# Kernel tuning notes

Hardware: AMD Instinct MI355X
Metric: run time of the kernel (lower is better)

## Reference

```python
import jax, jax.numpy as jnp
import numpy as np

AIR_TOKENS = jnp.array([102, 576, 3352], dtype=jnp.int32)
VOCAB = 3717
PS = 4  # patch size
L_CONN, L_PATCH, L_SMOOTH, L_SUPPORT = 0.5, 0.3, 0.1, 0.2


def _non_air(structure):
    # [B,X,Y,Z] bool: True where block is not air
    return ~jnp.isin(structure, AIR_TOKENS)


def connectivity_loss(structure):
    na = _non_air(structure).astype(jnp.float32)  # [B,X,Y,Z]
    p = jnp.pad(na, ((0, 0), (1, 1), (1, 1), (1, 1)))
    # 6-neighbor count (face adjacency), same math as the conv3d kernel
    neighbors = (p[:, :-2, 1:-1, 1:-1] + p[:, 2:, 1:-1, 1:-1]
                 + p[:, 1:-1, :-2, 1:-1] + p[:, 1:-1, 2:, 1:-1]
                 + p[:, 1:-1, 1:-1, :-2] + p[:, 1:-1, 1:-1, 2:])
    isolated = (neighbors == 0) & (na > 0)
    return isolated.astype(jnp.float32).sum() / (na.sum() + 1e-6)


def patch_consistency_loss(structure):
    B, X, Y, Z = structure.shape
    nx, ny, nz = X // PS, Y // PS, Z // PS
    num_patches = nx * ny * nz
    # [B, nx, PS, ny, PS, nz, PS] -> [B*num_patches, PS^3]
    patches = structure.reshape(B, nx, PS, ny, PS, nz, PS)
    patches = patches.transpose(0, 1, 3, 5, 2, 4, 6).reshape(B * num_patches, PS ** 3)
    P = B * num_patches
    # per-patch histogram over the vocab (fused replacement for unique/count loop)
    counts = jnp.zeros((P, VOCAB), jnp.float32)
    counts = counts.at[jnp.arange(P)[:, None], patches].add(1.0)
    counts = counts.at[:, AIR_TOKENS].set(0.0)  # drop air tokens
    s = counts.sum(-1, keepdims=True)
    probs = counts / jnp.maximum(s, 1.0)  # all-air patches -> probs 0 -> entropy 0
    entropy = -(probs * jnp.log(probs + 1e-10)).sum()
    return entropy / (B * num_patches + 1e-6)


def support_loss(structure):
    na = _non_air(structure)  # [B,X,Y,Z], Y is vertical
    support_below = jnp.concatenate(
        [jnp.ones_like(na[:, :, :1, :]), na[:, :, :-1, :]], axis=2)
    unsupported = na & ~support_below
    unsupported = unsupported.at[:, :, 0, :].set(False)  # exclude bottom layer
    return unsupported.astype(jnp.float32).sum() / (na.astype(jnp.float32).sum() + 1e-6)


def smoothness_loss(emb):
    # emb: [B, C, X, Y, Z]
    dx = jnp.abs(emb[:, :, 1:, :, :] - emb[:, :, :-1, :, :]).mean()
    dy = jnp.abs(emb[:, :, :, 1:, :] - emb[:, :, :, :-1, :]).mean()
    dz = jnp.abs(emb[:, :, :, :, 1:] - emb[:, :, :, :, :-1]).mean()
    return (dx + dy + dz) / 3.0


def setup_inputs() -> dict:
    key = jax.random.key(0)
    k1, k2 = jax.random.split(key)
    structure = jax.random.randint(k1, (64, 32, 32, 32), 0, VOCAB, dtype=jnp.int32)
    block_embeddings = jax.random.normal(k2, (64, 32, 32, 32, 32), dtype=jnp.float32)
    return {"structure": structure, "block_embeddings": block_embeddings}


def reference(structure, block_embeddings):
    l_conn = connectivity_loss(structure)
    l_patch = patch_consistency_loss(structure)
    l_support = support_loss(structure)
    l_smooth = smoothness_loss(block_embeddings)
    total = (L_CONN * l_conn + L_PATCH * l_patch
             + L_SMOOTH * l_smooth + L_SUPPORT * l_support)
    return (total, l_conn, l_patch, l_smooth, l_support)
```

## Files before the change

kernel.cpp:

```cpp
#include <hip/hip_runtime.h>


#define SM_BLOCKS 2048
#define ST_BLOCKS 1024
#define PA_BLOCKS 512
#define WS_DX  0
#define WS_DY  (SM_BLOCKS)
#define WS_DZ  (2 * SM_BLOCKS)
#define WS_ISO (3 * SM_BLOCKS)
#define WS_NA  (WS_ISO + ST_BLOCKS)
#define WS_UNS (WS_NA + ST_BLOCKS)
#define WS_ENT (WS_UNS + ST_BLOCKS)

__device__ __forceinline__ bool non_air(int t) {
    return !(t == 102 || t == 576 || t == 3352);
}

__device__ __forceinline__ double wave_red_d(double v) {
    #pragma unroll
    for (int off = 32; off > 0; off >>= 1) v += __shfl_down(v, off, 64);
    return v;
}
__device__ __forceinline__ float wave_red_f(float v) {
    #pragma unroll
    for (int off = 32; off > 0; off >>= 1) v += __shfl_down(v, off, 64);
    return v;
}
__device__ __forceinline__ int wave_red_i(int v) {
    #pragma unroll
    for (int off = 32; off > 0; off >>= 1) v += __shfl_down(v, off, 64);
    return v;
}

__device__ void smooth_body(const float4* __restrict__ e4,
                            double* __restrict__ part, int bid) {
    double adx = 0.0, ady = 0.0, adz = 0.0;
    const int stride = SM_BLOCKS * 256;
    for (int idx4 = bid * 256 + (int)threadIdx.x; idx4 < (1 << 24); idx4 += stride) {
        const int z4 = idx4 & 7;
        const int y = (idx4 >> 3) & 31;
        const int x = (idx4 >> 8) & 31;

        const float4 v = e4[idx4];

        const float nxt = __shfl_down(v.x, 1, 64);
        float dz = fabsf(v.y - v.x) + fabsf(v.z - v.y) + fabsf(v.w - v.z);
        if (z4 < 7) dz += fabsf(nxt - v.w);

        float dy = 0.0f;
        if (y < 31) {
            const float4 n = e4[idx4 + 8];
            dy = fabsf(n.x - v.x) + fabsf(n.y - v.y) + fabsf(n.z - v.z) + fabsf(n.w - v.w);
        }
        float dx = 0.0f;
        if (x < 31) {
            const float4 n = e4[idx4 + 256];
            dx = fabsf(n.x - v.x) + fabsf(n.y - v.y) + fabsf(n.z - v.z) + fabsf(n.w - v.w);
        }
        adx += dx; ady += dy; adz += dz;
    }

    adx = wave_red_d(adx); ady = wave_red_d(ady); adz = wave_red_d(adz);
    __shared__ double sm[3][4];
    const int lane = threadIdx.x & 63, wid = threadIdx.x >> 6;
    if (lane == 0) { sm[0][wid] = adx; sm[1][wid] = ady; sm[2][wid] = adz; }
    __syncthreads();
    if (threadIdx.x == 0) {
        part[WS_DX + bid] = sm[0][0] + sm[0][1] + sm[0][2] + sm[0][3];
        part[WS_DY + bid] = sm[1][0] + sm[1][1] + sm[1][2] + sm[1][3];
        part[WS_DZ + bid] = sm[2][0] + sm[2][1] + sm[2][2] + sm[2][3];
    }
}

__device__ void struct_body(const int* __restrict__ s,
                            double* __restrict__ part, int bid) {
    int iso = 0, nai = 0, unsup = 0;
    const int stride = ST_BLOCKS * 256;
    for (int idx = bid * 256 + (int)threadIdx.x; idx < (1 << 21); idx += stride) {
        const int z = idx & 31;
        const int y = (idx >> 5) & 31;
        const int x = (idx >> 10) & 31;
        const int t = s[idx];
        if (non_air(t)) {
            ++nai;
            int ncnt = 0;
            bool below = false;
            if (x > 0)  ncnt += non_air(s[idx - 1024]);
            if (x < 31) ncnt += non_air(s[idx + 1024]);
            if (y > 0)  { below = non_air(s[idx - 32]); ncnt += below; }
            if (y < 31) ncnt += non_air(s[idx + 32]);
            if (z > 0)  ncnt += non_air(s[idx - 1]);
            if (z < 31) ncnt += non_air(s[idx + 1]);
            iso += (ncnt == 0);
            unsup += (y > 0 && !below);
        }
    }
    iso = wave_red_i(iso); nai = wave_red_i(nai); unsup = wave_red_i(unsup);
    __shared__ int sm[3][4];
    const int lane = threadIdx.x & 63, wid = threadIdx.x >> 6;
    if (lane == 0) { sm[0][wid] = iso; sm[1][wid] = nai; sm[2][wid] = unsup; }
    __syncthreads();
    if (threadIdx.x == 0) {
        part[WS_ISO + bid] = (double)(sm[0][0] + sm[0][1] + sm[0][2] + sm[0][3]);
        part[WS_NA  + bid] = (double)(sm[1][0] + sm[1][1] + sm[1][2] + sm[1][3]);
        part[WS_UNS + bid] = (double)(sm[2][0] + sm[2][1] + sm[2][2] + sm[2][3]);
    }
}

__device__ void patch_body(const int* __restrict__ s,
                           double* __restrict__ part, int bid) {
    const int lane = threadIdx.x & 63, wid = threadIdx.x >> 6;
    const int gwave = bid * 4 + wid;
    const int nwaves = PA_BLOCKS * 4;
    const int px = lane >> 4, py = (lane >> 2) & 3, pz = lane & 3;

    float esum = 0.0f;
    for (int pid = gwave; pid < 32768; pid += nwaves) {
        const int b = pid >> 9;
        const int rem = pid & 511;
        const int ix = rem >> 6, iy = (rem >> 3) & 7, iz = rem & 7;
        const int x = ix * 4 + px, y = iy * 4 + py, z = iz * 4 + pz;

        const int t = s[((b * 32 + x) * 32 + y) * 32 + z];
        const bool na = non_air(t);
        const int scount = __popcll(__ballot(na));

        int c = 0, minj = 64;
        #pragma unroll 8
        for (int j = 0; j < 64; ++j) {
            const int tj = __shfl(t, j, 64);
            if (tj == t) { ++c; if (j < minj) minj = j; }
        }
        if (na && minj == lane) {
            const float p = (float)c / (float)(scount > 1 ? scount : 1);
            esum += -p * logf(p + 1e-10f);
        }
    }
    const float w = wave_red_f(esum);
    __shared__ float smp[4];
    if (lane == 0) smp[wid] = w;
    __syncthreads();
    if (threadIdx.x == 0)
        part[WS_ENT + bid] = (double)(smp[0] + smp[1] + smp[2] + smp[3]);
}

__global__ __launch_bounds__(256) void fused_kernel(const int* __restrict__ s,
                                                    const float4* __restrict__ e4,
                                                    double* __restrict__ part) {
    const int bid = blockIdx.x;
    if (bid < SM_BLOCKS) {
        smooth_body(e4, part, bid);
    } else if (bid < SM_BLOCKS + ST_BLOCKS) {
        struct_body(s, part, bid - SM_BLOCKS);
    } else {
        patch_body(s, part, bid - SM_BLOCKS - ST_BLOCKS);
    }
}

__global__ __launch_bounds__(256) void finalize_kernel(const double* __restrict__ part,
                                                       float* __restrict__ out) {
    __shared__ double sm[4];
    __shared__ double res[7];
    const int lane = threadIdx.x & 63, wid = threadIdx.x >> 6;
    const int base[7] = {WS_DX, WS_DY, WS_DZ, WS_ISO, WS_NA, WS_UNS, WS_ENT};
    const int len[7]  = {SM_BLOCKS, SM_BLOCKS, SM_BLOCKS, ST_BLOCKS, ST_BLOCKS, ST_BLOCKS, PA_BLOCKS};
    for (int k = 0; k < 7; ++k) {
        double a = 0.0;
        for (int i = threadIdx.x; i < len[k]; i += 256) a += part[base[k] + i];
        a = wave_red_d(a);
        if (lane == 0) sm[wid] = a;
        __syncthreads();
        if (threadIdx.x == 0) res[k] = sm[0] + sm[1] + sm[2] + sm[3];
        __syncthreads();
    }
    if (threadIdx.x == 0) {
        const double na = res[4];
        const double l_conn    = res[3] / (na + 1e-6);
        const double l_support = res[5] / (na + 1e-6);
        const double l_patch   = res[6] / (32768.0 + 1e-6);
        const double nd = 65011712.0;
        const double l_smooth  = (res[0] / nd + res[1] / nd + res[2] / nd) / 3.0;
        const double total = 0.5 * l_conn + 0.3 * l_patch + 0.1 * l_smooth + 0.2 * l_support;
        out[0] = (float)total;
        out[1] = (float)l_conn;
        out[2] = (float)l_patch;
        out[3] = (float)l_smooth;
        out[4] = (float)l_support;
    }
}

extern "C" void kernel_launch(void* const* d_in, const int* in_sizes, int n_in,
                              void* d_out, int out_size, void* d_ws, size_t ws_size,
                              hipStream_t stream) {
    const int*   s   = (const int*)d_in[0];
    const float* emb = (const float*)d_in[1];
    float* out   = (float*)d_out;
    double* part = (double*)d_ws;

    fused_kernel<<<SM_BLOCKS + ST_BLOCKS + PA_BLOCKS, 256, 0, stream>>>(
        s, (const float4*)emb, part);
    finalize_kernel<<<1, 256, 0, stream>>>(part, out);
}
```

Before: 437.6 us.

## Restructure smoothness loop with fixed trip count, float accumulators, and reordered block roles

The smoothness pass now uses a fixed 16-iteration loop that processes two float4 elements per iteration with branchless neighbor offsets. It reads the z-neighbor directly from memory instead of using a wave shuffle, and accumulates in float rather than double. The structure loop gets a constant trip count, and the structure and patch block counts are halved. Blocks are reordered so the slower patch and structure work is scheduled first. This should cut per-iteration index math and double-precision adds and give more memory-level parallelism, at the cost of float accumulation precision and fewer blocks for the integer passes.

```diff
diff --git a/kernel.cpp b/kernel.cpp
--- a/kernel.cpp
+++ b/kernel.cpp
@@ -2,8 +2,8 @@
 
 
 #define SM_BLOCKS 2048
-#define ST_BLOCKS 1024
-#define PA_BLOCKS 512
+#define ST_BLOCKS 512
+#define PA_BLOCKS 256
 #define WS_DX  0
 #define WS_DY  (SM_BLOCKS)
 #define WS_DZ  (2 * SM_BLOCKS)
@@ -32,38 +32,52 @@
     return v;
 }
 
-__device__ void smooth_body(const float4* __restrict__ e4,
+__device__ __forceinline__ float sad4(float4 a, float4 b) {
+    return fabsf(a.x - b.x) + fabsf(a.y - b.y) + fabsf(a.z - b.z) + fabsf(a.w - b.w);
+}
+
+__device__ void smooth_body(const float* __restrict__ e,
+                            const float4* __restrict__ e4,
                             double* __restrict__ part, int bid) {
-    double adx = 0.0, ady = 0.0, adz = 0.0;
-    const int stride = SM_BLOCKS * 256;
-    for (int idx4 = bid * 256 + (int)threadIdx.x; idx4 < (1 << 24); idx4 += stride) {
-        const int z4 = idx4 & 7;
-        const int y = (idx4 >> 3) & 31;
-        const int x = (idx4 >> 8) & 31;
-
-        const float4 v = e4[idx4];
-
-        const float nxt = __shfl_down(v.x, 1, 64);
-        float dz = fabsf(v.y - v.x) + fabsf(v.z - v.y) + fabsf(v.w - v.z);
-        if (z4 < 7) dz += fabsf(nxt - v.w);
-
-        float dy = 0.0f;
-        if (y < 31) {
-            const float4 n = e4[idx4 + 8];
-            dy = fabsf(n.x - v.x) + fabsf(n.y - v.y) + fabsf(n.z - v.z) + fabsf(n.w - v.w);
-        }
-        float dx = 0.0f;
-        if (x < 31) {
-            const float4 n = e4[idx4 + 256];
-            dx = fabsf(n.x - v.x) + fabsf(n.y - v.y) + fabsf(n.z - v.z) + fabsf(n.w - v.w);
-        }
-        adx += dx; ady += dy; adz += dz;
-    }
-
-    adx = wave_red_d(adx); ady = wave_red_d(ady); adz = wave_red_d(adz);
+    const int t0 = bid * 256 + (int)threadIdx.x;
+    const int z4 = t0 & 7;
+    const int y  = (t0 >> 3) & 31;
+    const int x  = (t0 >> 8) & 31;
+    const int   oy  = (y < 31) ? 8 : 0;
+    const int   ox  = (x < 31) ? 256 : 0;
+    const int   oz  = (z4 < 7) ? 4 : 0;
+    const float mzf = (z4 < 7) ? 1.0f : 0.0f;
+
+    float ax = 0.0f, ay = 0.0f, az = 0.0f;
+    const int S = 1 << 19;
+
+    #pragma unroll 1
+    for (int k = 0; k < 32; k += 2) {
+        const int i0 = t0 + k * S;
+        const int i1 = i0 + S;
+        const float4 v0 = e4[i0];
+        const float4 v1 = e4[i1];
+        const float4 py0 = e4[i0 + oy];
+        const float4 py1 = e4[i1 + oy];
+        const float4 px0 = e4[i0 + ox];
+        const float4 px1 = e4[i1 + ox];
+        const float  f0 = e[(i0 << 2) + oz];
+        const float  f1 = e[(i1 << 2) + oz];
+
+        az += fabsf(v0.y - v0.x) + fabsf(v0.z - v0.y) + fabsf(v0.w - v0.z)
+            + mzf * fabsf(f0 - v0.w);
+        az += fabsf(v1.y - v1.x) + fabsf(v1.z - v1.y) + fabsf(v1.w - v1.z)
+            + mzf * fabsf(f1 - v1.w);
+        ay += sad4(py0, v0) + sad4(py1, v1);
+        ax += sad4(px0, v0) + sad4(px1, v1);
+    }
+
+    double dxd = wave_red_d((double)ax);
+    double dyd = wave_red_d((double)ay);
+    double dzd = wave_red_d((double)az);
     __shared__ double sm[3][4];
     const int lane = threadIdx.x & 63, wid = threadIdx.x >> 6;
-    if (lane == 0) { sm[0][wid] = adx; sm[1][wid] = ady; sm[2][wid] = adz; }
+    if (lane == 0) { sm[0][wid] = dxd; sm[1][wid] = dyd; sm[2][wid] = dzd; }
     __syncthreads();
     if (threadIdx.x == 0) {
         part[WS_DX + bid] = sm[0][0] + sm[0][1] + sm[0][2] + sm[0][3];
@@ -74,12 +88,12 @@
 
 __device__ void struct_body(const int* __restrict__ s,
                             double* __restrict__ part, int bid) {
+    const int t0 = bid * 256 + (int)threadIdx.x;
+    const int z = t0 & 31, y = (t0 >> 5) & 31, x = (t0 >> 10) & 31;
     int iso = 0, nai = 0, unsup = 0;
-    const int stride = ST_BLOCKS * 256;
-    for (int idx = bid * 256 + (int)threadIdx.x; idx < (1 << 21); idx += stride) {
-        const int z = idx & 31;
-        const int y = (idx >> 5) & 31;
-        const int x = (idx >> 10) & 31;
+    #pragma unroll 2
+    for (int k = 0; k < 16; ++k) {
+        const int idx = t0 + (k << 17);
         const int t = s[idx];
         if (non_air(t)) {
             ++nai;
@@ -145,15 +159,16 @@
 }
 
 __global__ __launch_bounds__(256) void fused_kernel(const int* __restrict__ s,
+                                                    const float* __restrict__ e,
                                                     const float4* __restrict__ e4,
                                                     double* __restrict__ part) {
     const int bid = blockIdx.x;
-    if (bid < SM_BLOCKS) {
-        smooth_body(e4, part, bid);
-    } else if (bid < SM_BLOCKS + ST_BLOCKS) {
-        struct_body(s, part, bid - SM_BLOCKS);
+    if (bid < PA_BLOCKS) {
+        patch_body(s, part, bid);
+    } else if (bid < PA_BLOCKS + ST_BLOCKS) {
+        struct_body(s, part, bid - PA_BLOCKS);
     } else {
-        patch_body(s, part, bid - SM_BLOCKS - ST_BLOCKS);
+        smooth_body(e, e4, part, bid - PA_BLOCKS - ST_BLOCKS);
     }
 }
 
@@ -197,7 +212,7 @@
     float* out   = (float*)d_out;
     double* part = (double*)d_ws;
 
-    fused_kernel<<<SM_BLOCKS + ST_BLOCKS + PA_BLOCKS, 256, 0, stream>>>(
-        s, (const float4*)emb, part);
+    fused_kernel<<<PA_BLOCKS + ST_BLOCKS + SM_BLOCKS, 256, 0, stream>>>(
+        s, emb, (const float4*)emb, part);
     finalize_kernel<<<1, 256, 0, stream>>>(part, out);
 }
```

Measured after the change: 389.2 us. 11.1% less time.
